# Kernel optimization log

Hardware: AMD Instinct MI355X
Metric: run time of the kernel (lower is better)

The kernel has to match this reference:

```python
import jax, jax.numpy as jnp
import numpy as np

EMBED = 1024
HEADS = 16
HEAD_DIM = EMBED // HEADS


def setup_inputs() -> dict:
    key = jax.random.key(0)
    k1, k2, k3, k4, k5 = jax.random.split(key, 5)
    x = jax.random.normal(k1, (2, 2048, EMBED), dtype=jnp.float32)
    # torch nn.Linear params: weight [out, in], bias [out]; y = x @ W.T + b
    s_attn = 1.0 / np.sqrt(EMBED)
    w_attn = jax.random.uniform(k2, (3 * EMBED, EMBED), jnp.float32, -s_attn, s_attn)
    b_attn = jax.random.uniform(k3, (3 * EMBED,), jnp.float32, -s_attn, s_attn)
    w_proj = jax.random.uniform(k4, (EMBED, EMBED), jnp.float32, -s_attn, s_attn)
    b_proj = jax.random.uniform(k5, (EMBED,), jnp.float32, -s_attn, s_attn)
    return {"x": x, "w_attn": w_attn, "b_attn": b_attn, "w_proj": w_proj, "b_proj": b_proj}


def reference(x, w_attn, b_attn, w_proj, b_proj):
    B, S, D = x.shape
    qkv = x @ w_attn.T + b_attn                      # [B, S, 3D]
    q, k, v = jnp.split(qkv, 3, axis=-1)             # each [B, S, D]

    def heads(t):  # [B, S, D] -> [B, H, S, hd]
        return t.reshape(B, S, HEADS, HEAD_DIM).transpose(0, 2, 1, 3)

    q, k, v = heads(q), heads(k), heads(v)
    # Faithful to source: NO 1/sqrt(d) scaling, NO causal mask.
    w = jnp.einsum('bhqd,bhkd->bhqk', q, k)          # [B, H, S, S]
    w = jax.nn.softmax(w, axis=-1)
    a = jnp.einsum('bhqk,bhkd->bhqd', w, v)          # [B, H, S, hd]
    a = a.transpose(0, 2, 1, 3).reshape(B, S, D)     # merge heads
    return a @ w_proj.T + b_proj
```

## Files before the change

kernel.cpp:

```cpp
#include <hip/hip_runtime.h>
#include <hip/hip_bf16.h>
#include <stdint.h>
#include <math.h>


typedef __attribute__((ext_vector_type(2))) float f32x2;
typedef __attribute__((ext_vector_type(4))) float f32x4;
typedef __attribute__((ext_vector_type(16))) float f32x16;
typedef __attribute__((ext_vector_type(8))) short bf16x8;

static __device__ __forceinline__ unsigned short f2bf(float f) {
    unsigned u = __float_as_uint(f);
    u += 0x7FFFu + ((u >> 16) & 1u);
    return (unsigned short)(u >> 16);
}
static __device__ __forceinline__ unsigned cvt_pk_bf16(float a, float b) {
    unsigned r;
    asm("v_cvt_pk_bf16_f32 %0, %1, %2" : "=v"(r) : "v"(a), "v"(b));
    return r;
}
static __device__ __forceinline__ float fexp2(float x) {
    float r;
    asm("v_exp_f32 %0, %1" : "=v"(r) : "v"(x));
    return r;
}

typedef const __attribute__((address_space(1))) unsigned int* gas_ptr;
typedef __attribute__((address_space(3))) unsigned int* las_ptr;
static __device__ __forceinline__ void gload_lds16(const void* g, void* l) {
    __builtin_amdgcn_global_load_lds((gas_ptr)g, (las_ptr)l, 16, 0, 0);
}

__global__ void conv_all_kernel(const float* __restrict__ x,
                                const float* __restrict__ wa,
                                const float* __restrict__ wp,
                                unsigned short* __restrict__ x1,
                                unsigned short* __restrict__ w1a,
                                unsigned short* __restrict__ wpb) {
    int i = blockIdx.x * blockDim.x + threadIdx.x;
    int stride = gridDim.x * blockDim.x;
    for (; i < 2097152; i += stride) {
        const float* s; unsigned short* d; int j;
        if (i < 1048576)      { s = x;  d = x1;  j = i; }
        else if (i < 1835008) { s = wa; d = w1a; j = i - 1048576; }
        else                  { s = wp; d = wpb; j = i - 1835008; }
        float4 v = ((const float4*)s)[j];
        ushort4 o;
        o.x = f2bf(v.x); o.y = f2bf(v.y); o.z = f2bf(v.z); o.w = f2bf(v.w);
        ((ushort4*)d)[j] = o;
    }
}

__global__ __launch_bounds__(256, 2) void gemm_qkv_kernel(
    const unsigned short* __restrict__ A,
    const unsigned short* __restrict__ Bw,
    const float* __restrict__ bias,
    unsigned short* __restrict__ q1,
    unsigned short* __restrict__ k1,
    unsigned short* __restrict__ vT,
    int N, int K)
{
    __shared__ __align__(16) unsigned char lds[34816];
    const int t  = threadIdx.x;
    const int lane = t & 63;
    const int w  = t >> 6;
    const int wr = w >> 1, wc = w & 1;
    const int lg = lane >> 4, ll = lane & 15;

    const int gx = gridDim.x;
    const int flat = blockIdx.y * gx + blockIdx.x;
    const int cpx = (gx * gridDim.y) >> 3;
    const int swz = (flat & 7) * cpx + (flat >> 3);
    const int m0 = (swz / gx) * 128;
    const int n0 = (swz % gx) * 128;

    f32x4 acc[4][4] = {};

    const int srow  = t >> 3;
    const int sslot = t & 7;
    const unsigned short* Abase[4];
    const unsigned short* Bbase[4];
#pragma unroll
    for (int ci = 0; ci < 4; ++ci) {
        int r  = ci * 32 + srow;
        int cg = sslot ^ (r & 7);
        Abase[ci] = A  + (size_t)(m0 + r) * K + cg * 8;
        Bbase[ci] = Bw + (size_t)(n0 + r) * K + cg * 8;
    }

    for (int k0 = 0; k0 < K; k0 += 64) {
#pragma unroll
        for (int ci = 0; ci < 4; ++ci)
            gload_lds16(Abase[ci] + k0, lds + ci*4096 + (t>>6)*1024);
#pragma unroll
        for (int ci = 0; ci < 4; ++ci)
            gload_lds16(Bbase[ci] + k0, lds + 16384 + ci*4096 + (t>>6)*1024);
        __syncthreads();

        bf16x8 af[4][2], bfr[4][2];
#pragma unroll
        for (int mt = 0; mt < 4; ++mt)
#pragma unroll
            for (int kc = 0; kc < 2; ++kc) {
                int row = wr*64 + mt*16 + ll;
                int cg  = (4*kc + lg) ^ (row & 7);
                af[mt][kc] = *(const bf16x8*)(lds + row*128 + cg*16);
            }
#pragma unroll
        for (int nt = 0; nt < 4; ++nt)
#pragma unroll
            for (int kc = 0; kc < 2; ++kc) {
                int row = wc*64 + nt*16 + ll;
                int cg  = (4*kc + lg) ^ (row & 7);
                bfr[nt][kc] = *(const bf16x8*)(lds + 16384 + row*128 + cg*16);
            }
#pragma unroll
        for (int kc = 0; kc < 2; ++kc)
#pragma unroll
            for (int mt = 0; mt < 4; ++mt)
#pragma unroll
                for (int nt = 0; nt < 4; ++nt)
                    acc[mt][nt] = __builtin_amdgcn_mfma_f32_16x16x32_bf16(
                        af[mt][kc], bfr[nt][kc], acc[mt][nt], 0, 0, 0);
        __syncthreads();
    }

    const int TYPE = n0 >> 10;
    unsigned short* l16 = (unsigned short*)lds;
#pragma unroll
    for (int mt = 0; mt < 4; ++mt)
#pragma unroll
      for (int nt = 0; nt < 4; ++nt)
#pragma unroll
        for (int r = 0; r < 4; ++r) {
            int mp = wr*64 + mt*16 + 4*lg + r;
            int np = wc*64 + nt*16 + ll;
            float v = acc[mt][nt][r] + bias[n0 + np];
            if (TYPE == 0) v *= 1.44269504f;
            unsigned short h16 = f2bf(v);
            if (TYPE == 2) l16[np*136 + mp] = h16;
            else           l16[mp*136 + np] = h16;
        }
    __syncthreads();
    {
        const int r2 = t >> 1, half = t & 1;
        const unsigned short* src = l16 + r2*136 + half*64;
        unsigned short* dst;
        if (TYPE == 2) {
            int n = n0 + r2;
            int h = (n >> 6) & 15, d = n & 63;
            int bb = m0 >> 11;
            dst = vT + ((size_t)(bb*16 + h)*64 + d)*2048 + (m0 & 2047) + half*64;
        } else {
            int m = m0 + r2;
            int bb = m >> 11, s = m & 2047;
            int h = ((n0 + half*64) >> 6) & 15;
            dst = (TYPE == 0 ? q1 : k1) + ((size_t)(bb*16 + h)*2048 + s)*64;
        }
#pragma unroll
        for (int j = 0; j < 8; ++j)
            *(uint4*)(dst + j*8) = *(const uint4*)(src + j*8);
    }
}

__global__ __launch_bounds__(256, 2) void gemm_proj_kernel(
    const unsigned short* __restrict__ A,
    const unsigned short* __restrict__ Bw,
    const float* __restrict__ bias,
    float* __restrict__ outp)
{
    __shared__ __align__(16) unsigned char lds[24576];
    const int t  = threadIdx.x;
    const int lane = t & 63;
    const int w  = t >> 6;
    const int lg = lane >> 4, ll = lane & 15;

    const int flat = blockIdx.y * 16 + blockIdx.x;
    const int swz = (flat & 7) * 64 + (flat >> 3);
    const int m0 = (swz >> 4) * 128;
    const int n0 = (swz & 15) * 64;

    f32x4 acc[2][4] = {};

    const int srow  = t >> 3;
    const int sslot = t & 7;
    const unsigned short* Abase[4];
    const unsigned short* Bbase[2];
#pragma unroll
    for (int ci = 0; ci < 4; ++ci) {
        int r  = ci * 32 + srow;
        int cg = sslot ^ (r & 7);
        Abase[ci] = A + (size_t)(m0 + r) * 1024 + cg * 8;
    }
#pragma unroll
    for (int ci = 0; ci < 2; ++ci) {
        int r  = ci * 32 + srow;
        int cg = sslot ^ (r & 7);
        Bbase[ci] = Bw + (size_t)(n0 + r) * 1024 + cg * 8;
    }

    for (int k0 = 0; k0 < 1024; k0 += 64) {
#pragma unroll
        for (int ci = 0; ci < 4; ++ci)
            gload_lds16(Abase[ci] + k0, lds + ci*4096 + w*1024);
#pragma unroll
        for (int ci = 0; ci < 2; ++ci)
            gload_lds16(Bbase[ci] + k0, lds + 16384 + ci*4096 + w*1024);
        __syncthreads();

        bf16x8 af[2][2], bfr[4][2];
#pragma unroll
        for (int mt = 0; mt < 2; ++mt)
#pragma unroll
            for (int kc = 0; kc < 2; ++kc) {
                int row = w*32 + mt*16 + ll;
                int cg  = (4*kc + lg) ^ (row & 7);
                af[mt][kc] = *(const bf16x8*)(lds + row*128 + cg*16);
            }
#pragma unroll
        for (int nt = 0; nt < 4; ++nt)
#pragma unroll
            for (int kc = 0; kc < 2; ++kc) {
                int row = nt*16 + ll;
                int cg  = (4*kc + lg) ^ (row & 7);
                bfr[nt][kc] = *(const bf16x8*)(lds + 16384 + row*128 + cg*16);
            }
#pragma unroll
        for (int kc = 0; kc < 2; ++kc)
#pragma unroll
            for (int mt = 0; mt < 2; ++mt)
#pragma unroll
                for (int nt = 0; nt < 4; ++nt)
                    acc[mt][nt] = __builtin_amdgcn_mfma_f32_16x16x32_bf16(
                        af[mt][kc], bfr[nt][kc], acc[mt][nt], 0, 0, 0);
        __syncthreads();
    }

#pragma unroll
    for (int mt = 0; mt < 2; ++mt)
#pragma unroll
      for (int nt = 0; nt < 4; ++nt)
#pragma unroll
        for (int r = 0; r < 4; ++r) {
            int m = m0 + w*32 + mt*16 + 4*lg + r;
            int n = n0 + nt*16 + ll;
            outp[(size_t)m * 1024 + n] = acc[mt][nt][r] + bias[n];
        }
}

__global__ __launch_bounds__(512, 2) void attn_kernel(
    const unsigned short* __restrict__ q1,
    const unsigned short* __restrict__ k1,
    const unsigned short* __restrict__ vT,
    unsigned short* __restrict__ aout)
{
    __shared__ __align__(16) unsigned char lds[65536];
    const int t = threadIdx.x, lane = t & 63, w = t >> 6;
    const int hi = lane >> 5, lq = lane & 31, l7 = lane & 7;
    const int gp = w >> 2, sw = w & 3;

    const int D  = blockIdx.x;
    const int bh = (D & 7) + ((D >> 6) << 3);
    const int qb = (D >> 3) & 7;
    const int q0 = qb * 256 + sw * 64;

    bf16x8 qfA[4], qfB[4];
    {
        const unsigned short* qpA = q1 + ((size_t)bh*2048 + q0 + lq)*64 + hi*8;
        const unsigned short* qpB = qpA + 32*64;
#pragma unroll
        for (int ks = 0; ks < 4; ++ks) {
            qfA[ks] = *(const bf16x8*)(qpA + ks*16);
            qfB[ks] = *(const bf16x8*)(qpB + ks*16);
        }
    }

    f32x16 oA0 = {}, oA1 = {}, oB0 = {}, oB1 = {};
    f32x2 lra = {0.f, 0.f}, lrb = {0.f, 0.f};
    const f32x16 fz = {};

    const int sr = t >> 3, ss = t & 7;
    const int scg = ss ^ (sr & 7);
    const int psr = (sr & 51) | ((sr & 4) << 1) | ((sr & 8) >> 1);
    const unsigned short* Ksrc = k1 + ((size_t)bh*2048 + psr)*64 + scg*8;
    const unsigned short* Vsrc = vT + ((size_t)bh*64 + sr)*2048 + scg*8;
    const int sdst = w*1024;

    unsigned char* fb0 = lds + gp*8192 + lq*128 + (((0 + hi) ^ l7) << 4);
    unsigned char* fb1 = lds + gp*8192 + lq*128 + (((2 + hi) ^ l7) << 4);
    unsigned char* fb2 = lds + gp*8192 + lq*128 + (((4 + hi) ^ l7) << 4);
    unsigned char* fb3 = lds + gp*8192 + lq*128 + (((6 + hi) ^ l7) << 4);

    gload_lds16(Ksrc,        lds + sdst);
    gload_lds16(Ksrc + 4096, lds + 8192 + sdst);
    gload_lds16(Vsrc,        lds + 32768 + sdst);
    gload_lds16(Vsrc + 64,   lds + 32768 + 8192 + sdst);
    __syncthreads();

#define SOFT_PACK(SV, PA, PB, LR)                                             \
    {                                                                         \
        float e0 =fexp2(SV[0]),  e1 =fexp2(SV[1]),  e2 =fexp2(SV[2]);         \
        float e3 =fexp2(SV[3]),  e4 =fexp2(SV[4]),  e5 =fexp2(SV[5]);         \
        float e6 =fexp2(SV[6]),  e7 =fexp2(SV[7]),  e8 =fexp2(SV[8]);         \
        float e9 =fexp2(SV[9]),  e10=fexp2(SV[10]), e11=fexp2(SV[11]);        \
        float e12=fexp2(SV[12]), e13=fexp2(SV[13]), e14=fexp2(SV[14]);        \
        float e15=fexp2(SV[15]);                                              \
        union { unsigned u[4]; bf16x8 v; } A_, B_;                            \
        A_.u[0]=cvt_pk_bf16(e0,e1);   A_.u[1]=cvt_pk_bf16(e2,e3);             \
        A_.u[2]=cvt_pk_bf16(e4,e5);   A_.u[3]=cvt_pk_bf16(e6,e7);             \
        B_.u[0]=cvt_pk_bf16(e8,e9);   B_.u[1]=cvt_pk_bf16(e10,e11);           \
        B_.u[2]=cvt_pk_bf16(e12,e13); B_.u[3]=cvt_pk_bf16(e14,e15);           \
        PA = A_.v; PB = B_.v;                                                 \
        f32x2 p0 = {e0,e1};   p0 += (f32x2){e2,e3};                           \
        p0 += (f32x2){e4,e5};   p0 += (f32x2){e6,e7};                         \
        p0 += (f32x2){e8,e9};   p0 += (f32x2){e10,e11};                       \
        p0 += (f32x2){e12,e13}; p0 += (f32x2){e14,e15};                       \
        LR += p0;                                                             \
    }

#define STEP(PAR)                                                             \
    {                                                                         \
        f32x16 sA0, sA1, sB0, sB1;                                            \
        bf16x8 kf;                                                            \
        __builtin_amdgcn_s_setprio(1);                                        \
        kf = *(const bf16x8*)(fb0 + (PAR)*16384);                             \
        sA0 = __builtin_amdgcn_mfma_f32_32x32x16_bf16(kf, qfA[0], fz, 0,0,0); \
        sB0 = __builtin_amdgcn_mfma_f32_32x32x16_bf16(kf, qfB[0], fz, 0,0,0); \
        kf = *(const bf16x8*)(fb0 + (PAR)*16384 + 4096);                      \
        sA1 = __builtin_amdgcn_mfma_f32_32x32x16_bf16(kf, qfA[0], fz, 0,0,0); \
        sB1 = __builtin_amdgcn_mfma_f32_32x32x16_bf16(kf, qfB[0], fz, 0,0,0); \
        kf = *(const bf16x8*)(fb1 + (PAR)*16384);                             \
        sA0 = __builtin_amdgcn_mfma_f32_32x32x16_bf16(kf, qfA[1], sA0, 0,0,0);\
        sB0 = __builtin_amdgcn_mfma_f32_32x32x16_bf16(kf, qfB[1], sB0, 0,0,0);\
        kf = *(const bf16x8*)(fb1 + (PAR)*16384 + 4096);                      \
        sA1 = __builtin_amdgcn_mfma_f32_32x32x16_bf16(kf, qfA[1], sA1, 0,0,0);\
        sB1 = __builtin_amdgcn_mfma_f32_32x32x16_bf16(kf, qfB[1], sB1, 0,0,0);\
        kf = *(const bf16x8*)(fb2 + (PAR)*16384);                             \
        sA0 = __builtin_amdgcn_mfma_f32_32x32x16_bf16(kf, qfA[2], sA0, 0,0,0);\
        sB0 = __builtin_amdgcn_mfma_f32_32x32x16_bf16(kf, qfB[2], sB0, 0,0,0);\
        kf = *(const bf16x8*)(fb2 + (PAR)*16384 + 4096);                      \
        sA1 = __builtin_amdgcn_mfma_f32_32x32x16_bf16(kf, qfA[2], sA1, 0,0,0);\
        sB1 = __builtin_amdgcn_mfma_f32_32x32x16_bf16(kf, qfB[2], sB1, 0,0,0);\
        kf = *(const bf16x8*)(fb3 + (PAR)*16384);                             \
        sA0 = __builtin_amdgcn_mfma_f32_32x32x16_bf16(kf, qfA[3], sA0, 0,0,0);\
        sB0 = __builtin_amdgcn_mfma_f32_32x32x16_bf16(kf, qfB[3], sB0, 0,0,0);\
        kf = *(const bf16x8*)(fb3 + (PAR)*16384 + 4096);                      \
        sA1 = __builtin_amdgcn_mfma_f32_32x32x16_bf16(kf, qfA[3], sA1, 0,0,0);\
        sB1 = __builtin_amdgcn_mfma_f32_32x32x16_bf16(kf, qfB[3], sB1, 0,0,0);\
        __builtin_amdgcn_s_setprio(0);                                        \
        bf16x8 pa0, pa1, pa2, pa3;                                            \
        bf16x8 vf;                                                            \
        SOFT_PACK(sA0, pa0, pa1, lra)                                         \
        SOFT_PACK(sA1, pa2, pa3, lra)                                         \
        __builtin_amdgcn_s_setprio(1);                                        \
        vf = *(const bf16x8*)(fb0 + (PAR)*16384 + 32768);                     \
        oA0 = __builtin_amdgcn_mfma_f32_32x32x16_bf16(pa0, vf, oA0, 0,0,0);   \
        vf = *(const bf16x8*)(fb0 + (PAR)*16384 + 32768 + 4096);              \
        oA1 = __builtin_amdgcn_mfma_f32_32x32x16_bf16(pa0, vf, oA1, 0,0,0);   \
        vf = *(const bf16x8*)(fb1 + (PAR)*16384 + 32768);                     \
        oA0 = __builtin_amdgcn_mfma_f32_32x32x16_bf16(pa1, vf, oA0, 0,0,0);   \
        vf = *(const bf16x8*)(fb1 + (PAR)*16384 + 32768 + 4096);              \
        oA1 = __builtin_amdgcn_mfma_f32_32x32x16_bf16(pa1, vf, oA1, 0,0,0);   \
        vf = *(const bf16x8*)(fb2 + (PAR)*16384 + 32768);                     \
        oA0 = __builtin_amdgcn_mfma_f32_32x32x16_bf16(pa2, vf, oA0, 0,0,0);   \
        vf = *(const bf16x8*)(fb2 + (PAR)*16384 + 32768 + 4096);              \
        oA1 = __builtin_amdgcn_mfma_f32_32x32x16_bf16(pa2, vf, oA1, 0,0,0);   \
        vf = *(const bf16x8*)(fb3 + (PAR)*16384 + 32768);                     \
        oA0 = __builtin_amdgcn_mfma_f32_32x32x16_bf16(pa3, vf, oA0, 0,0,0);   \
        vf = *(const bf16x8*)(fb3 + (PAR)*16384 + 32768 + 4096);              \
        oA1 = __builtin_amdgcn_mfma_f32_32x32x16_bf16(pa3, vf, oA1, 0,0,0);   \
        __builtin_amdgcn_s_setprio(0);                                        \
        SOFT_PACK(sB0, pa0, pa1, lrb)                                         \
        SOFT_PACK(sB1, pa2, pa3, lrb)                                         \
        __builtin_amdgcn_s_setprio(1);                                        \
        vf = *(const bf16x8*)(fb0 + (PAR)*16384 + 32768);                     \
        oB0 = __builtin_amdgcn_mfma_f32_32x32x16_bf16(pa0, vf, oB0, 0,0,0);   \
        vf = *(const bf16x8*)(fb0 + (PAR)*16384 + 32768 + 4096);              \
        oB1 = __builtin_amdgcn_mfma_f32_32x32x16_bf16(pa0, vf, oB1, 0,0,0);   \
        vf = *(const bf16x8*)(fb1 + (PAR)*16384 + 32768);                     \
        oB0 = __builtin_amdgcn_mfma_f32_32x32x16_bf16(pa1, vf, oB0, 0,0,0);   \
        vf = *(const bf16x8*)(fb1 + (PAR)*16384 + 32768 + 4096);              \
        oB1 = __builtin_amdgcn_mfma_f32_32x32x16_bf16(pa1, vf, oB1, 0,0,0);   \
        vf = *(const bf16x8*)(fb2 + (PAR)*16384 + 32768);                     \
        oB0 = __builtin_amdgcn_mfma_f32_32x32x16_bf16(pa2, vf, oB0, 0,0,0);   \
        vf = *(const bf16x8*)(fb2 + (PAR)*16384 + 32768 + 4096);              \
        oB1 = __builtin_amdgcn_mfma_f32_32x32x16_bf16(pa2, vf, oB1, 0,0,0);   \
        vf = *(const bf16x8*)(fb3 + (PAR)*16384 + 32768);                     \
        oB0 = __builtin_amdgcn_mfma_f32_32x32x16_bf16(pa3, vf, oB0, 0,0,0);   \
        vf = *(const bf16x8*)(fb3 + (PAR)*16384 + 32768 + 4096);              \
        oB1 = __builtin_amdgcn_mfma_f32_32x32x16_bf16(pa3, vf, oB1, 0,0,0);   \
        __builtin_amdgcn_s_setprio(0);                                        \
    }

    for (int sp = 0; sp < 8; ++sp) {
        {
            const size_t T = 4*(size_t)sp + 2;
            gload_lds16(Ksrc + T*4096,        lds + 16384 + sdst);
            gload_lds16(Ksrc + T*4096 + 4096, lds + 24576 + sdst);
            gload_lds16(Vsrc + T*64,          lds + 32768 + 16384 + sdst);
            gload_lds16(Vsrc + T*64 + 64,     lds + 32768 + 24576 + sdst);
            STEP(0)
            __syncthreads();
        }
        {
            if (sp < 7) {
                const size_t T = 4*(size_t)sp + 4;
                gload_lds16(Ksrc + T*4096,        lds + sdst);
                gload_lds16(Ksrc + T*4096 + 4096, lds + 8192 + sdst);
                gload_lds16(Vsrc + T*64,          lds + 32768 + sdst);
                gload_lds16(Vsrc + T*64 + 64,     lds + 32768 + 8192 + sdst);
            }
            STEP(1)
            __syncthreads();
        }
    }
#undef STEP
#undef SOFT_PACK

    float la = lra[0] + lra[1];  la += __shfl_xor(la, 32);
    float lb = lrb[0] + lrb[1];  lb += __shfl_xor(lb, 32);

    float* mb = (float*)lds;
    const int slot = (sw << 6) + lane;
    const int bb = bh >> 4, h = bh & 15;

    if (gp == 1) {
        float* p = mb + slot * 36;
#pragma unroll
        for (int c = 0; c < 4; ++c) {
            f32x4 v0 = { oA0[4*c], oA0[4*c+1], oA0[4*c+2], oA0[4*c+3] };
            *(f32x4*)(p + 4*c) = v0;
            f32x4 v1 = { oA1[4*c], oA1[4*c+1], oA1[4*c+2], oA1[4*c+3] };
            *(f32x4*)(p + 16 + 4*c) = v1;
        }
        p[32] = la;
    }
    __syncthreads();
    if (gp == 0) {
        const float* p = mb + slot * 36;
#pragma unroll
        for (int c = 0; c < 4; ++c) {
            f32x4 v0 = *(const f32x4*)(p + 4*c);
            oA0[4*c] += v0[0]; oA0[4*c+1] += v0[1];
            oA0[4*c+2] += v0[2]; oA0[4*c+3] += v0[3];
            f32x4 v1 = *(const f32x4*)(p + 16 + 4*c);
            oA1[4*c] += v1[0]; oA1[4*c+1] += v1[1];
            oA1[4*c+2] += v1[2]; oA1[4*c+3] += v1[3];
        }
        la += p[32];
        const float linv_own = 1.0f / la;
#pragma unroll
        for (int r = 0; r < 16; ++r) {
            int qrow = (r & 3) + 8*(r >> 2) + 4*hi;
            float linv = __shfl(linv_own, qrow);
            size_t srow = q0 + qrow;
            aout[((size_t)(bb*2048 + srow)*16 + h)*64 + lq]      = f2bf(oA0[r] * linv);
            aout[((size_t)(bb*2048 + srow)*16 + h)*64 + 32 + lq] = f2bf(oA1[r] * linv);
        }
    }
    __syncthreads();

    if (gp == 1) {
        float* p = mb + slot * 36;
#pragma unroll
        for (int c = 0; c < 4; ++c) {
            f32x4 v0 = { oB0[4*c], oB0[4*c+1], oB0[4*c+2], oB0[4*c+3] };
            *(f32x4*)(p + 4*c) = v0;
            f32x4 v1 = { oB1[4*c], oB1[4*c+1], oB1[4*c+2], oB1[4*c+3] };
            *(f32x4*)(p + 16 + 4*c) = v1;
        }
        p[32] = lb;
    }
    __syncthreads();
    if (gp == 0) {
        const float* p = mb + slot * 36;
#pragma unroll
        for (int c = 0; c < 4; ++c) {
            f32x4 v0 = *(const f32x4*)(p + 4*c);
            oB0[4*c] += v0[0]; oB0[4*c+1] += v0[1];
            oB0[4*c+2] += v0[2]; oB0[4*c+3] += v0[3];
            f32x4 v1 = *(const f32x4*)(p + 16 + 4*c);
            oB1[4*c] += v1[0]; oB1[4*c+1] += v1[1];
            oB1[4*c+2] += v1[2]; oB1[4*c+3] += v1[3];
        }
        lb += p[32];
        const float linv_own = 1.0f / lb;
#pragma unroll
        for (int r = 0; r < 16; ++r) {
            int qrow = (r & 3) + 8*(r >> 2) + 4*hi;
            float linv = __shfl(linv_own, qrow);
            size_t srow = q0 + 32 + qrow;
            aout[((size_t)(bb*2048 + srow)*16 + h)*64 + lq]      = f2bf(oB0[r] * linv);
            aout[((size_t)(bb*2048 + srow)*16 + h)*64 + 32 + lq] = f2bf(oB1[r] * linv);
        }
    }
}

extern "C" void kernel_launch(void* const* d_in, const int* in_sizes, int n_in,
                              void* d_out, int out_size, void* d_ws, size_t ws_size,
                              hipStream_t stream) {
    const float* x      = (const float*)d_in[0];
    const float* w_attn = (const float*)d_in[1];
    const float* b_attn = (const float*)d_in[2];
    const float* w_proj = (const float*)d_in[3];
    const float* b_proj = (const float*)d_in[4];
    float* out = (float*)d_out;

    unsigned char* ws = (unsigned char*)d_ws;
    unsigned short* x1  = (unsigned short*)(ws);
    unsigned short* w1a = (unsigned short*)(ws + (size_t)8*1024*1024);
    unsigned short* wpb = (unsigned short*)(ws + (size_t)14*1024*1024);
    unsigned short* q1  = (unsigned short*)(ws + (size_t)16*1024*1024);
    unsigned short* k1  = (unsigned short*)(ws + (size_t)24*1024*1024);
    unsigned short* vT  = (unsigned short*)(ws + (size_t)32*1024*1024);
    unsigned short* ab  = (unsigned short*)(ws + (size_t)40*1024*1024);

    conv_all_kernel<<<2048, 256, 0, stream>>>(x, w_attn, w_proj, x1, w1a, wpb);

    gemm_qkv_kernel<<<dim3(24, 32), 256, 0, stream>>>(
        x1, w1a, b_attn, q1, k1, vT, 3072, 1024);

    attn_kernel<<<256, 512, 0, stream>>>(q1, k1, vT, ab);

    gemm_proj_kernel<<<dim3(16, 32), 256, 0, stream>>>(ab, wpb, b_proj, out);
}
```

Before: 102.5 us.

## Retile QKV GEMM to 256x192 tiles with double-buffered LDS and 512 threads

Restructures the QKV projection GEMM to use 256x192 output tiles with 8 waves (512 threads), a 32-wide K step and double-buffered LDS so the next stage's global-to-LDS loads overlap the MFMA work. The grid shrinks to 256 blocks, one per CU-sized wave of work, and raises MFMA priority during the compute section. The LDS-staged coalesced epilogue is replaced by direct scalar bf16 stores from accumulators. The V-transpose store in particular becomes strided, which may cost write efficiency.

```diff
diff --git a/kernel.cpp b/kernel.cpp
--- a/kernel.cpp
+++ b/kernel.cpp
@@ -51,116 +51,101 @@
     }
 }
 
-__global__ __launch_bounds__(256, 2) void gemm_qkv_kernel(
+__global__ __launch_bounds__(512, 2) void gemm_qkv_kernel(
     const unsigned short* __restrict__ A,
     const unsigned short* __restrict__ Bw,
     const float* __restrict__ bias,
     unsigned short* __restrict__ q1,
     unsigned short* __restrict__ k1,
-    unsigned short* __restrict__ vT,
-    int N, int K)
+    unsigned short* __restrict__ vT)
 {
-    __shared__ __align__(16) unsigned char lds[34816];
-    const int t  = threadIdx.x;
+    __shared__ __align__(16) unsigned char lds[65536];
+    const int t = threadIdx.x;
     const int lane = t & 63;
     const int w  = t >> 6;
-    const int wr = w >> 1, wc = w & 1;
+    const int wm = w >> 2, wn = w & 3;
     const int lg = lane >> 4, ll = lane & 15;
 
-    const int gx = gridDim.x;
-    const int flat = blockIdx.y * gx + blockIdx.x;
-    const int cpx = (gx * gridDim.y) >> 3;
-    const int swz = (flat & 7) * cpx + (flat >> 3);
-    const int m0 = (swz / gx) * 128;
-    const int n0 = (swz % gx) * 128;
-
-    f32x4 acc[4][4] = {};
-
-    const int srow  = t >> 3;
-    const int sslot = t & 7;
-    const unsigned short* Abase[4];
-    const unsigned short* Bbase[4];
-#pragma unroll
-    for (int ci = 0; ci < 4; ++ci) {
-        int r  = ci * 32 + srow;
-        int cg = sslot ^ (r & 7);
-        Abase[ci] = A  + (size_t)(m0 + r) * K + cg * 8;
-        Bbase[ci] = Bw + (size_t)(n0 + r) * K + cg * 8;
-    }
-
-    for (int k0 = 0; k0 < K; k0 += 64) {
-#pragma unroll
-        for (int ci = 0; ci < 4; ++ci)
-            gload_lds16(Abase[ci] + k0, lds + ci*4096 + (t>>6)*1024);
-#pragma unroll
-        for (int ci = 0; ci < 4; ++ci)
-            gload_lds16(Bbase[ci] + k0, lds + 16384 + ci*4096 + (t>>6)*1024);
+    const int flat = blockIdx.y * 16 + blockIdx.x;
+    const int swz = (flat & 7) * 32 + (flat >> 3);
+    const int m0 = (swz >> 4) * 256;
+    const int n0 = (swz & 15) * 192;
+
+    f32x4 acc[8][3] = {};
+
+    const int rA = t >> 2, sA = t & 3;
+    const unsigned short* Asrc1 = A + (size_t)(m0 + rA) * 1024 + (sA ^ (rA & 3)) * 8;
+    const unsigned short* Asrc2 = Asrc1 + (size_t)128 * 1024;
+    const unsigned short* Bsrc1 = Bw + (size_t)(n0 + rA) * 1024 + (sA ^ (rA & 3)) * 8;
+    const int rc = (rA < 64) ? rA + 128 : 191;
+    const unsigned short* Bsrc2 = Bw + (size_t)(n0 + rc) * 1024 + (sA ^ (rc & 3)) * 8;
+    const int sdst = w * 1024;
+
+#define QKV_STAGE(IT, B)                                                      \
+    {                                                                         \
+        const size_t ko = (size_t)(IT) * 32;                                  \
+        gload_lds16(Asrc1 + ko, lds + (B)*16384 + sdst);                      \
+        gload_lds16(Asrc2 + ko, lds + (B)*16384 + 8192 + sdst);               \
+        gload_lds16(Bsrc1 + ko, lds + 32768 + (B)*16384 + sdst);              \
+        gload_lds16(Bsrc2 + ko, lds + 32768 + (B)*16384 + 8192 + sdst);       \
+    }
+
+    QKV_STAGE(0, 0)
+    __syncthreads();
+
+    for (int it = 0; it < 32; ++it) {
+        const int buf = it & 1;
+        if (it < 31) QKV_STAGE(it + 1, buf ^ 1)
+
+        bf16x8 af[8], bf[3];
+#pragma unroll
+        for (int mt = 0; mt < 8; ++mt) {
+            int row = wm*128 + mt*16 + ll;
+            af[mt] = *(const bf16x8*)(lds + buf*16384 + row*64
+                                      + ((lg ^ (row & 3)) << 4));
+        }
+#pragma unroll
+        for (int nt = 0; nt < 3; ++nt) {
+            int row = wn*48 + nt*16 + ll;
+            bf[nt] = *(const bf16x8*)(lds + 32768 + buf*16384 + row*64
+                                      + ((lg ^ (row & 3)) << 4));
+        }
+        __builtin_amdgcn_s_setprio(1);
+#pragma unroll
+        for (int mt = 0; mt < 8; ++mt)
+#pragma unroll
+            for (int nt = 0; nt < 3; ++nt)
+                acc[mt][nt] = __builtin_amdgcn_mfma_f32_16x16x32_bf16(
+                    af[mt], bf[nt], acc[mt][nt], 0, 0, 0);
+        __builtin_amdgcn_s_setprio(0);
         __syncthreads();
-
-        bf16x8 af[4][2], bfr[4][2];
-#pragma unroll
-        for (int mt = 0; mt < 4; ++mt)
-#pragma unroll
-            for (int kc = 0; kc < 2; ++kc) {
-                int row = wr*64 + mt*16 + ll;
-                int cg  = (4*kc + lg) ^ (row & 7);
-                af[mt][kc] = *(const bf16x8*)(lds + row*128 + cg*16);
+    }
+#undef QKV_STAGE
+
+#pragma unroll
+    for (int mt = 0; mt < 8; ++mt)
+#pragma unroll
+      for (int nt = 0; nt < 3; ++nt)
+#pragma unroll
+        for (int r = 0; r < 4; ++r) {
+            int m = m0 + wm*128 + mt*16 + 4*lg + r;
+            int n = n0 + wn*48 + nt*16 + ll;
+            float v = acc[mt][nt][r] + bias[n];
+            int bb = m >> 11;
+            int s  = m & 2047;
+            int which = n >> 10;
+            int h  = (n >> 6) & 15;
+            int d  = n & 63;
+            int bh = bb * 16 + h;
+            if (which == 2) {
+                vT[((size_t)bh * 64 + d) * 2048 + s] = f2bf(v);
+            } else {
+                float vq = (which == 0) ? v * 1.44269504f : v;
+                unsigned short* dp = (which == 0 ? q1 : k1)
+                                   + ((size_t)bh * 2048 + s) * 64 + d;
+                *dp = f2bf(vq);
             }
-#pragma unroll
-        for (int nt = 0; nt < 4; ++nt)
-#pragma unroll
-            for (int kc = 0; kc < 2; ++kc) {
-                int row = wc*64 + nt*16 + ll;
-                int cg  = (4*kc + lg) ^ (row & 7);
-                bfr[nt][kc] = *(const bf16x8*)(lds + 16384 + row*128 + cg*16);
-            }
-#pragma unroll
-        for (int kc = 0; kc < 2; ++kc)
-#pragma unroll
-            for (int mt = 0; mt < 4; ++mt)
-#pragma unroll
-                for (int nt = 0; nt < 4; ++nt)
-                    acc[mt][nt] = __builtin_amdgcn_mfma_f32_16x16x32_bf16(
-                        af[mt][kc], bfr[nt][kc], acc[mt][nt], 0, 0, 0);
-        __syncthreads();
-    }
-
-    const int TYPE = n0 >> 10;
-    unsigned short* l16 = (unsigned short*)lds;
-#pragma unroll
-    for (int mt = 0; mt < 4; ++mt)
-#pragma unroll
-      for (int nt = 0; nt < 4; ++nt)
-#pragma unroll
-        for (int r = 0; r < 4; ++r) {
-            int mp = wr*64 + mt*16 + 4*lg + r;
-            int np = wc*64 + nt*16 + ll;
-            float v = acc[mt][nt][r] + bias[n0 + np];
-            if (TYPE == 0) v *= 1.44269504f;
-            unsigned short h16 = f2bf(v);
-            if (TYPE == 2) l16[np*136 + mp] = h16;
-            else           l16[mp*136 + np] = h16;
-        }
-    __syncthreads();
-    {
-        const int r2 = t >> 1, half = t & 1;
-        const unsigned short* src = l16 + r2*136 + half*64;
-        unsigned short* dst;
-        if (TYPE == 2) {
-            int n = n0 + r2;
-            int h = (n >> 6) & 15, d = n & 63;
-            int bb = m0 >> 11;
-            dst = vT + ((size_t)(bb*16 + h)*64 + d)*2048 + (m0 & 2047) + half*64;
-        } else {
-            int m = m0 + r2;
-            int bb = m >> 11, s = m & 2047;
-            int h = ((n0 + half*64) >> 6) & 15;
-            dst = (TYPE == 0 ? q1 : k1) + ((size_t)(bb*16 + h)*2048 + s)*64;
-        }
-#pragma unroll
-        for (int j = 0; j < 8; ++j)
-            *(uint4*)(dst + j*8) = *(const uint4*)(src + j*8);
-    }
+        }
 }
 
 __global__ __launch_bounds__(256, 2) void gemm_proj_kernel(
@@ -517,8 +502,8 @@
 
     conv_all_kernel<<<2048, 256, 0, stream>>>(x, w_attn, w_proj, x1, w1a, wpb);
 
-    gemm_qkv_kernel<<<dim3(24, 32), 256, 0, stream>>>(
-        x1, w1a, b_attn, q1, k1, vT, 3072, 1024);
+    gemm_qkv_kernel<<<dim3(16, 16), 512, 0, stream>>>(
+        x1, w1a, b_attn, q1, k1, vT);
 
     attn_kernel<<<256, 512, 0, stream>>>(q1, k1, vT, ab);
 
```

Result: slower. 116.8 us (+14.0%).
